# Optimization experiments

Hardware: AMD Instinct MI355X
Metric: run time of the kernel (lower is better)

## Reference

```python
import jax, jax.numpy as jnp
import numpy as np

DIM = 1024
HEADS = 16
HEAD_DIM = DIM // HEADS
HIDDEN = 4 * DIM
EPS = 1e-5


def _layernorm(x, g, b):
    mu = jnp.mean(x, axis=-1, keepdims=True)
    var = jnp.mean(jnp.square(x - mu), axis=-1, keepdims=True)
    return (x - mu) * jax.lax.rsqrt(var + EPS) * g + b


def setup_inputs() -> dict:
    key = jax.random.key(0)
    ks = jax.random.split(key, 10)
    s = lambda fan_in: 1.0 / np.sqrt(fan_in)
    return {
        "x": jax.random.normal(ks[0], (8, 2048, DIM), dtype=jnp.float32),
        # weights stored (in, out): y = x @ W + b
        "w_qkv": jax.random.uniform(ks[1], (DIM, 3 * DIM), minval=-s(DIM), maxval=s(DIM)),
        "b_qkv": jnp.zeros((3 * DIM,), jnp.float32),
        "w_proj": jax.random.uniform(ks[2], (DIM, DIM), minval=-s(DIM), maxval=s(DIM)),
        "b_proj": jnp.zeros((DIM,), jnp.float32),
        "w_fc1": jax.random.uniform(ks[3], (DIM, HIDDEN), minval=-s(DIM), maxval=s(DIM)),
        "b_fc1": jnp.zeros((HIDDEN,), jnp.float32),
        "w_fc2": jax.random.uniform(ks[4], (HIDDEN, DIM), minval=-s(HIDDEN), maxval=s(HIDDEN)),
        "b_fc2": jnp.zeros((DIM,), jnp.float32),
        "g1": jnp.ones((DIM,), jnp.float32),
        "be1": jnp.zeros((DIM,), jnp.float32),
        "g2": jnp.ones((DIM,), jnp.float32),
        "be2": jnp.zeros((DIM,), jnp.float32),
    }


def reference(x, w_qkv, b_qkv, w_proj, b_proj, w_fc1, b_fc1, w_fc2, b_fc2, g1, be1, g2, be2):
    B, N, D = x.shape
    scale = HEAD_DIM ** -0.5

    # --- attention (faithful to source: q,k,v kept as (B,N,H,hd), no head permute) ---
    h = _layernorm(x, g1, be1)
    qkv = (h @ w_qkv + b_qkv).reshape(B, N, 3, HEADS, HEAD_DIM)
    q, k, v = qkv[:, :, 0], qkv[:, :, 1], qkv[:, :, 2]
    # (B,N,H,hd) @ (B,N,hd,H) -> per-token head-head scores (B,N,H,H)
    attn = jnp.einsum('bnhd,bngd->bnhg', q, k) * scale
    attn = jax.nn.softmax(attn, axis=-1)
    o = jnp.einsum('bnhg,bngd->bnhd', attn, v)          # (B,N,H,hd)
    o = jnp.transpose(o, (0, 2, 1, 3)).reshape(B, N, D)  # source's transpose(1,2).reshape
    x = x + o @ w_proj + b_proj

    # --- MLP ---
    h = _layernorm(x, g2, be2)
    h = jax.nn.gelu(h @ w_fc1 + b_fc1, approximate=False)  # torch nn.GELU default = exact
    x = x + h @ w_fc2 + b_fc2
    return x
```

## Files before the change

### kernel.cpp

```cpp
#include <hip/hip_runtime.h>
#include <hip/hip_bf16.h>
#include <math.h>

typedef unsigned short u16;
typedef __attribute__((ext_vector_type(8))) short bf16x8;
typedef __attribute__((ext_vector_type(4))) float f32x4;

#define NTOK 16384
#define LN_EPS 1e-5f

static __device__ __forceinline__ u16 f2bf(float f) {
  unsigned u = __float_as_uint(f);
  u += 0x7fffu + ((u >> 16) & 1u);
  return (u16)(u >> 16);
}
static __device__ __forceinline__ float bf2f(u16 u) {
  return __uint_as_float(((unsigned)u) << 16);
}

__global__ __launch_bounds__(256) void transpose_bf16(const float* __restrict__ in,
                                                      u16* __restrict__ out,
                                                      int K, int N) {
  __shared__ float tile[32][33];
  int n0 = blockIdx.x * 32, k0 = blockIdx.y * 32;
  int tx = threadIdx.x, ty = threadIdx.y;
#pragma unroll
  for (int i = 0; i < 32; i += 8)
    tile[ty + i][tx] = in[(size_t)(k0 + ty + i) * N + n0 + tx];
  __syncthreads();
#pragma unroll
  for (int i = 0; i < 32; i += 8)
    out[(size_t)(n0 + ty + i) * K + k0 + tx] = f2bf(tile[tx][ty + i]);
}

__global__ __launch_bounds__(256) void ln_bf16(const float* __restrict__ x,
                                               const float* __restrict__ g,
                                               const float* __restrict__ be,
                                               u16* __restrict__ out) {
  __shared__ float red[8];
  int row = blockIdx.x;
  int t = threadIdx.x;
  float4 v = ((const float4*)(x + (size_t)row * 1024))[t];
  float s = v.x + v.y + v.z + v.w;
  float ss = v.x * v.x + v.y * v.y + v.z * v.z + v.w * v.w;
#pragma unroll
  for (int i = 1; i < 64; i <<= 1) {
    s += __shfl_xor(s, i);
    ss += __shfl_xor(ss, i);
  }
  int lane = t & 63, wid = t >> 6;
  if (lane == 0) { red[wid] = s; red[4 + wid] = ss; }
  __syncthreads();
  s = red[0] + red[1] + red[2] + red[3];
  ss = red[4] + red[5] + red[6] + red[7];
  float mu = s * (1.0f / 1024.0f);
  float var = ss * (1.0f / 1024.0f) - mu * mu;
  float rs = rsqrtf(var + LN_EPS);
  float4 gv = ((const float4*)g)[t];
  float4 bv = ((const float4*)be)[t];
  ushort4 o;
  o.x = f2bf((v.x - mu) * rs * gv.x + bv.x);
  o.y = f2bf((v.y - mu) * rs * gv.y + bv.y);
  o.z = f2bf((v.z - mu) * rs * gv.z + bv.z);
  o.w = f2bf((v.w - mu) * rs * gv.w + bv.w);
  ((ushort4*)(out + (size_t)row * 1024))[t] = o;
}

__global__ __launch_bounds__(256) void attn_kernel(const u16* __restrict__ qkv,
                                                   u16* __restrict__ operm) {
  int tok = (blockIdx.x << 2) + (threadIdx.x >> 6);
  int lane = threadIdx.x & 63;
  int h = lane >> 2, sub = lane & 3;
  const u16* base = qkv + (size_t)tok * 3072;
  const u16* qp = base + h * 64;
  const u16* kp = base + 1024;
  const u16* vp = base + 2048;

  float sc[4] = {0.f, 0.f, 0.f, 0.f};
#pragma unroll
  for (int d0 = 0; d0 < 64; d0 += 8) {
    bf16x8 q8 = *(const bf16x8*)(qp + d0);
    float qf[8];
#pragma unroll
    for (int j = 0; j < 8; ++j) qf[j] = bf2f((u16)q8[j]);
#pragma unroll
    for (int gi = 0; gi < 4; ++gi) {
      bf16x8 k8 = *(const bf16x8*)(kp + (sub * 4 + gi) * 64 + d0);
#pragma unroll
      for (int j = 0; j < 8; ++j) sc[gi] += qf[j] * bf2f((u16)k8[j]);
    }
  }
  const float scale = 0.125f;
#pragma unroll
  for (int gi = 0; gi < 4; ++gi) sc[gi] *= scale;
  float mx = fmaxf(fmaxf(sc[0], sc[1]), fmaxf(sc[2], sc[3]));
  mx = fmaxf(mx, __shfl_xor(mx, 1));
  mx = fmaxf(mx, __shfl_xor(mx, 2));
  float p[4], sum = 0.f;
#pragma unroll
  for (int gi = 0; gi < 4; ++gi) { p[gi] = expf(sc[gi] - mx); sum += p[gi]; }
  sum += __shfl_xor(sum, 1);
  sum += __shfl_xor(sum, 2);
  float inv = 1.0f / sum;
#pragma unroll
  for (int gi = 0; gi < 4; ++gi) p[gi] *= inv;

  float pall[16];
#pragma unroll
  for (int g = 0; g < 16; ++g)
    pall[g] = __shfl(p[g & 3], (lane & ~3) | (g >> 2));

  float o[16];
#pragma unroll
  for (int j = 0; j < 16; ++j) o[j] = 0.f;
#pragma unroll
  for (int g = 0; g < 16; ++g) {
    bf16x8 v0 = *(const bf16x8*)(vp + g * 64 + sub * 16);
    bf16x8 v1 = *(const bf16x8*)(vp + g * 64 + sub * 16 + 8);
#pragma unroll
    for (int j = 0; j < 8; ++j) {
      o[j] += pall[g] * bf2f((u16)v0[j]);
      o[8 + j] += pall[g] * bf2f((u16)v1[j]);
    }
  }
  int b = tok >> 11, n = tok & 2047;
  size_t off = ((size_t)b << 21) + (size_t)(h * 128 + (n >> 4)) * 1024 +
               (size_t)((n & 15) * 64 + sub * 16);
  bf16x8 w0, w1;
#pragma unroll
  for (int j = 0; j < 8; ++j) {
    w0[j] = (short)f2bf(o[j]);
    w1[j] = (short)f2bf(o[8 + j]);
  }
  *(bf16x8*)(operm + off) = w0;
  *(bf16x8*)(operm + off + 8) = w1;
}

template <int EPI>
__global__ __launch_bounds__(512, 2) void gemm256(const u16* __restrict__ A,
                                                  const u16* __restrict__ BT,
                                                  const float* __restrict__ bias,
                                                  const float* __restrict__ res,
                                                  void* __restrict__ outp,
                                                  int M, int N, int K) {
  __shared__ u16 As[2][256 * 64];
  __shared__ u16 Bs[2][256 * 64];
  const int tid = threadIdx.x;
  const int wid = tid >> 6, lane = tid & 63;
  const int wm = wid >> 2, wn = wid & 3;
  const int lrow = lane & 15, lhi = lane >> 4;

  const int nbx = gridDim.x;
  const int nwg = nbx * gridDim.y;
  const int wg = blockIdx.y * nbx + blockIdx.x;
  const int cpx = nwg >> 3;
  const int swz = (wg & 7) * cpx + (wg >> 3);
  const int bn = swz % nbx, bm = swz / nbx;

  const int NT = K >> 6;

  const int r8 = tid >> 3;
  const int k8s = (tid & 7) ^ (r8 & 7);
  const u16* pA = A + (size_t)(bm * 256 + r8) * K + k8s * 8;
  const u16* pB = BT + (size_t)(bn * 256 + r8) * K + k8s * 8;
  const int ldsbase = wid * 512;

  auto stage2 = [&](int t, int pair) {
    if (t >= NT) return;
    const u16* g = (pair < 2 ? pA : pB) + (size_t)t * 64;
    u16* l = (pair < 2 ? &As[t & 1][0] : &Bs[t & 1][0]);
#pragma unroll
    for (int j = 0; j < 2; ++j) {
      const int i = (pair & 1) * 2 + j;
      __builtin_amdgcn_global_load_lds(
          (const __attribute__((address_space(1))) void*)(g + (size_t)i * 64 * K),
          (__attribute__((address_space(3))) void*)(l + i * 4096 + ldsbase), 16, 0, 0);
    }
  };

  stage2(0, 0); stage2(0, 1); stage2(0, 2); stage2(0, 3);
  stage2(1, 0); stage2(1, 1); stage2(1, 2);

  f32x4 acc[8][4] = {};
  const int rbA = wm * 128 + lrow;
  const int rbB = wn * 64 + lrow;
  const int sl0 = ((0 + lhi) ^ (lrow & 7)) << 3;
  const int sl1 = ((4 + lhi) ^ (lrow & 7)) << 3;

  for (int t = 0; t < NT; ++t) {
    if (t == NT - 1) {
      asm volatile("s_waitcnt vmcnt(0)" ::: "memory");
    } else {
      asm volatile("s_waitcnt vmcnt(6)" ::: "memory");
    }
    stage2(t + 1, 3);
    __builtin_amdgcn_s_barrier();
    __builtin_amdgcn_sched_barrier(0);

    const u16* Ab = &As[t & 1][0];
    const u16* Bb = &Bs[t & 1][0];
    bf16x8 af[8][2], bf[4][2];
#pragma unroll
    for (int n = 0; n < 4; ++n) {
      bf[n][0] = *(const bf16x8*)(Bb + (rbB + n * 16) * 64 + sl0);
      bf[n][1] = *(const bf16x8*)(Bb + (rbB + n * 16) * 64 + sl1);
    }
#pragma unroll
    for (int m = 0; m < 8; ++m) {
      af[m][0] = *(const bf16x8*)(Ab + (rbA + m * 16) * 64 + sl0);
      af[m][1] = *(const bf16x8*)(Ab + (rbA + m * 16) * 64 + sl1);
    }
    __builtin_amdgcn_s_setprio(1);
#pragma unroll
    for (int mm = 0; mm < 2; ++mm)
#pragma unroll
      for (int n = 0; n < 4; ++n) {
        acc[mm][n] = __builtin_amdgcn_mfma_f32_16x16x32_bf16(af[mm][0], bf[n][0], acc[mm][n], 0, 0, 0);
        acc[mm][n] = __builtin_amdgcn_mfma_f32_16x16x32_bf16(af[mm][1], bf[n][1], acc[mm][n], 0, 0, 0);
      }
    __builtin_amdgcn_s_setprio(0);

    asm volatile("s_waitcnt lgkmcnt(0)" ::: "memory");
    __builtin_amdgcn_s_barrier();
    __builtin_amdgcn_sched_barrier(0);

    stage2(t + 2, 0);
    __builtin_amdgcn_s_setprio(1);
#pragma unroll
    for (int mm = 2; mm < 4; ++mm)
#pragma unroll
      for (int n = 0; n < 4; ++n) {
        acc[mm][n] = __builtin_amdgcn_mfma_f32_16x16x32_bf16(af[mm][0], bf[n][0], acc[mm][n], 0, 0, 0);
        acc[mm][n] = __builtin_amdgcn_mfma_f32_16x16x32_bf16(af[mm][1], bf[n][1], acc[mm][n], 0, 0, 0);
      }
    __builtin_amdgcn_s_setprio(0);
    stage2(t + 2, 1);
    __builtin_amdgcn_s_setprio(1);
#pragma unroll
    for (int mm = 4; mm < 6; ++mm)
#pragma unroll
      for (int n = 0; n < 4; ++n) {
        acc[mm][n] = __builtin_amdgcn_mfma_f32_16x16x32_bf16(af[mm][0], bf[n][0], acc[mm][n], 0, 0, 0);
        acc[mm][n] = __builtin_amdgcn_mfma_f32_16x16x32_bf16(af[mm][1], bf[n][1], acc[mm][n], 0, 0, 0);
      }
    __builtin_amdgcn_s_setprio(0);
    stage2(t + 2, 2);
    __builtin_amdgcn_s_setprio(1);
#pragma unroll
    for (int mm = 6; mm < 8; ++mm)
#pragma unroll
      for (int n = 0; n < 4; ++n) {
        acc[mm][n] = __builtin_amdgcn_mfma_f32_16x16x32_bf16(af[mm][0], bf[n][0], acc[mm][n], 0, 0, 0);
        acc[mm][n] = __builtin_amdgcn_mfma_f32_16x16x32_bf16(af[mm][1], bf[n][1], acc[mm][n], 0, 0, 0);
      }
    __builtin_amdgcn_s_setprio(0);
  }

  const size_t crow0 = (size_t)bm * 256 + (size_t)wm * 128;
  const int ccol0 = bn * 256 + wn * 64;
#pragma unroll
  for (int n = 0; n < 4; ++n) {
    const int col = ccol0 + n * 16 + lrow;
    const float bb = bias[col];
#pragma unroll
    for (int m = 0; m < 8; ++m) {
#pragma unroll
      for (int r = 0; r < 4; ++r) {
        const size_t row = crow0 + m * 16 + lhi * 4 + r;
        const size_t idx = row * (size_t)N + col;
        float val = acc[m][n][r] + bb;
        if (EPI == 1 || EPI == 3) val += res[idx];
        if (EPI == 2) val = 0.5f * val * (1.0f + erff(val * 0.70710678118654752f));
        if (EPI == 0 || EPI == 2)
          ((u16*)outp)[idx] = f2bf(val);
        else
          ((float*)outp)[idx] = val;
      }
    }
  }
}

extern "C" void kernel_launch(void* const* d_in, const int* in_sizes, int n_in,
                              void* d_out, int out_size, void* d_ws, size_t ws_size,
                              hipStream_t stream) {
  const float* x = (const float*)d_in[0];
  const float* w_qkv = (const float*)d_in[1];
  const float* b_qkv = (const float*)d_in[2];
  const float* w_proj = (const float*)d_in[3];
  const float* b_proj = (const float*)d_in[4];
  const float* w_fc1 = (const float*)d_in[5];
  const float* b_fc1 = (const float*)d_in[6];
  const float* w_fc2 = (const float*)d_in[7];
  const float* b_fc2 = (const float*)d_in[8];
  const float* g1 = (const float*)d_in[9];
  const float* be1 = (const float*)d_in[10];
  const float* g2 = (const float*)d_in[11];
  const float* be2 = (const float*)d_in[12];
  float* out = (float*)d_out;

  char* ws = (char*)d_ws;
  u16* wqkvT = (u16*)ws; ws += (size_t)3072 * 1024 * 2;
  u16* wprojT = (u16*)ws; ws += (size_t)1024 * 1024 * 2;
  u16* wfc1T = (u16*)ws; ws += (size_t)4096 * 1024 * 2;
  u16* wfc2T = (u16*)ws; ws += (size_t)1024 * 4096 * 2;
  u16* hbuf = (u16*)ws; ws += (size_t)NTOK * 1024 * 2;
  u16* big = (u16*)ws;

  transpose_bf16<<<dim3(3072 / 32, 1024 / 32), dim3(32, 8), 0, stream>>>(w_qkv, wqkvT, 1024, 3072);
  transpose_bf16<<<dim3(1024 / 32, 1024 / 32), dim3(32, 8), 0, stream>>>(w_proj, wprojT, 1024, 1024);
  transpose_bf16<<<dim3(4096 / 32, 1024 / 32), dim3(32, 8), 0, stream>>>(w_fc1, wfc1T, 1024, 4096);
  transpose_bf16<<<dim3(1024 / 32, 4096 / 32), dim3(32, 8), 0, stream>>>(w_fc2, wfc2T, 4096, 1024);

  ln_bf16<<<NTOK, 256, 0, stream>>>(x, g1, be1, hbuf);

  gemm256<0><<<dim3(3072 / 256, NTOK / 256), 512, 0, stream>>>(hbuf, wqkvT, b_qkv, nullptr, big, NTOK, 3072, 1024);

  attn_kernel<<<NTOK / 4, 256, 0, stream>>>(big, hbuf);

  gemm256<1><<<dim3(1024 / 256, NTOK / 256), 512, 0, stream>>>(hbuf, wprojT, b_proj, x, out, NTOK, 1024, 1024);

  ln_bf16<<<NTOK, 256, 0, stream>>>(out, g2, be2, hbuf);

  gemm256<2><<<dim3(4096 / 256, NTOK / 256), 512, 0, stream>>>(hbuf, wfc1T, b_fc1, nullptr, big, NTOK, 4096, 1024);

  gemm256<3><<<dim3(1024 / 256, NTOK / 256), 512, 0, stream>>>(big, wfc2T, b_fc2, out, out, NTOK, 1024, 4096);
}
```

Before: 674.5 us.

## Restructure GEMM main loop to simple double-buffer with interleaved LDS reads

Replaces the split, staggered prefetch schedule (tile t+2 loaded in quarters between MFMA groups, with a one-and-a-half-stage lead) with a plain double-buffered scheme: all A and B loads for tile t+1 are issued at the top of each iteration, followed by a vmcnt(8) wait. Operand fragments are now read from LDS per k-half and per pair of M rows right before their MFMAs instead of being loaded all at once. This lowers register pressure from holding every fragment, but it shortens prefetch distance and spreads LDS reads into the MFMA stream, which may expose more global-load latency.

```diff
diff --git a/kernel.cpp b/kernel.cpp
--- a/kernel.cpp
+++ b/kernel.cpp
@@ -165,95 +165,69 @@
   const u16* pB = BT + (size_t)(bn * 256 + r8) * K + k8s * 8;
   const int ldsbase = wid * 512;
 
-  auto stage2 = [&](int t, int pair) {
+  auto stageAll = [&](int t) {
     if (t >= NT) return;
-    const u16* g = (pair < 2 ? pA : pB) + (size_t)t * 64;
-    u16* l = (pair < 2 ? &As[t & 1][0] : &Bs[t & 1][0]);
-#pragma unroll
-    for (int j = 0; j < 2; ++j) {
-      const int i = (pair & 1) * 2 + j;
+    const size_t koff = (size_t)t * 64;
+    u16* la = &As[t & 1][0];
+    u16* lb = &Bs[t & 1][0];
+#pragma unroll
+    for (int i = 0; i < 4; ++i) {
       __builtin_amdgcn_global_load_lds(
-          (const __attribute__((address_space(1))) void*)(g + (size_t)i * 64 * K),
-          (__attribute__((address_space(3))) void*)(l + i * 4096 + ldsbase), 16, 0, 0);
+          (const __attribute__((address_space(1))) void*)(pA + koff + (size_t)i * 64 * K),
+          (__attribute__((address_space(3))) void*)(la + i * 4096 + ldsbase), 16, 0, 0);
+    }
+#pragma unroll
+    for (int i = 0; i < 4; ++i) {
+      __builtin_amdgcn_global_load_lds(
+          (const __attribute__((address_space(1))) void*)(pB + koff + (size_t)i * 64 * K),
+          (__attribute__((address_space(3))) void*)(lb + i * 4096 + ldsbase), 16, 0, 0);
     }
   };
 
-  stage2(0, 0); stage2(0, 1); stage2(0, 2); stage2(0, 3);
-  stage2(1, 0); stage2(1, 1); stage2(1, 2);
+  stageAll(0);
 
   f32x4 acc[8][4] = {};
   const int rbA = wm * 128 + lrow;
   const int rbB = wn * 64 + lrow;
-  const int sl0 = ((0 + lhi) ^ (lrow & 7)) << 3;
-  const int sl1 = ((4 + lhi) ^ (lrow & 7)) << 3;
+  const int swz8 = (lrow & 7);
 
   for (int t = 0; t < NT; ++t) {
-    if (t == NT - 1) {
+    stageAll(t + 1);
+    if (t + 1 < NT) {
+      asm volatile("s_waitcnt vmcnt(8)" ::: "memory");
+    } else {
       asm volatile("s_waitcnt vmcnt(0)" ::: "memory");
-    } else {
-      asm volatile("s_waitcnt vmcnt(6)" ::: "memory");
-    }
-    stage2(t + 1, 3);
+    }
     __builtin_amdgcn_s_barrier();
     __builtin_amdgcn_sched_barrier(0);
 
     const u16* Ab = &As[t & 1][0];
     const u16* Bb = &Bs[t & 1][0];
-    bf16x8 af[8][2], bf[4][2];
-#pragma unroll
-    for (int n = 0; n < 4; ++n) {
-      bf[n][0] = *(const bf16x8*)(Bb + (rbB + n * 16) * 64 + sl0);
-      bf[n][1] = *(const bf16x8*)(Bb + (rbB + n * 16) * 64 + sl1);
-    }
-#pragma unroll
-    for (int m = 0; m < 8; ++m) {
-      af[m][0] = *(const bf16x8*)(Ab + (rbA + m * 16) * 64 + sl0);
-      af[m][1] = *(const bf16x8*)(Ab + (rbA + m * 16) * 64 + sl1);
-    }
-    __builtin_amdgcn_s_setprio(1);
-#pragma unroll
-    for (int mm = 0; mm < 2; ++mm)
-#pragma unroll
-      for (int n = 0; n < 4; ++n) {
-        acc[mm][n] = __builtin_amdgcn_mfma_f32_16x16x32_bf16(af[mm][0], bf[n][0], acc[mm][n], 0, 0, 0);
-        acc[mm][n] = __builtin_amdgcn_mfma_f32_16x16x32_bf16(af[mm][1], bf[n][1], acc[mm][n], 0, 0, 0);
+#pragma unroll
+    for (int s = 0; s < 2; ++s) {
+      const int sl = ((s * 4 + lhi) ^ swz8) << 3;
+      bf16x8 bfv[4];
+#pragma unroll
+      for (int n = 0; n < 4; ++n)
+        bfv[n] = *(const bf16x8*)(Bb + (rbB + n * 16) * 64 + sl);
+#pragma unroll
+      for (int q = 0; q < 4; ++q) {
+        bf16x8 a0 = *(const bf16x8*)(Ab + (rbA + (2 * q) * 16) * 64 + sl);
+        bf16x8 a1 = *(const bf16x8*)(Ab + (rbA + (2 * q + 1) * 16) * 64 + sl);
+        __builtin_amdgcn_s_setprio(1);
+#pragma unroll
+        for (int n = 0; n < 4; ++n) {
+          acc[2 * q][n] = __builtin_amdgcn_mfma_f32_16x16x32_bf16(a0, bfv[n], acc[2 * q][n], 0, 0, 0);
+          acc[2 * q + 1][n] = __builtin_amdgcn_mfma_f32_16x16x32_bf16(a1, bfv[n], acc[2 * q + 1][n], 0, 0, 0);
+        }
+        __builtin_amdgcn_s_setprio(0);
       }
-    __builtin_amdgcn_s_setprio(0);
+    }
 
     asm volatile("s_waitcnt lgkmcnt(0)" ::: "memory");
+    __builtin_amdgcn_sched_barrier(0);
     __builtin_amdgcn_s_barrier();
     __builtin_amdgcn_sched_barrier(0);
-
-    stage2(t + 2, 0);
-    __builtin_amdgcn_s_setprio(1);
-#pragma unroll
-    for (int mm = 2; mm < 4; ++mm)
-#pragma unroll
-      for (int n = 0; n < 4; ++n) {
-        acc[mm][n] = __builtin_amdgcn_mfma_f32_16x16x32_bf16(af[mm][0], bf[n][0], acc[mm][n], 0, 0, 0);
-        acc[mm][n] = __builtin_amdgcn_mfma_f32_16x16x32_bf16(af[mm][1], bf[n][1], acc[mm][n], 0, 0, 0);
-      }
-    __builtin_amdgcn_s_setprio(0);
-    stage2(t + 2, 1);
-    __builtin_amdgcn_s_setprio(1);
-#pragma unroll
-    for (int mm = 4; mm < 6; ++mm)
-#pragma unroll
-      for (int n = 0; n < 4; ++n) {
-        acc[mm][n] = __builtin_amdgcn_mfma_f32_16x16x32_bf16(af[mm][0], bf[n][0], acc[mm][n], 0, 0, 0);
-        acc[mm][n] = __builtin_amdgcn_mfma_f32_16x16x32_bf16(af[mm][1], bf[n][1], acc[mm][n], 0, 0, 0);
-      }
-    __builtin_amdgcn_s_setprio(0);
-    stage2(t + 2, 2);
-    __builtin_amdgcn_s_setprio(1);
-#pragma unroll
-    for (int mm = 6; mm < 8; ++mm)
-#pragma unroll
-      for (int n = 0; n < 4; ++n) {
-        acc[mm][n] = __builtin_amdgcn_mfma_f32_16x16x32_bf16(af[mm][0], bf[n][0], acc[mm][n], 0, 0, 0);
-        acc[mm][n] = __builtin_amdgcn_mfma_f32_16x16x32_bf16(af[mm][1], bf[n][1], acc[mm][n], 0, 0, 0);
-      }
-    __builtin_amdgcn_s_setprio(0);
   }
 
   const size_t crow0 = (size_t)bm * 256 + (size_t)wm * 128;
```

After: 745.4 us. +10.5%, slower.
